# Kernel tuning notes

Hardware: AMD Instinct MI355X
Metric: run time of the kernel (lower is better)

## Reference

```python
import jax, jax.numpy as jnp
import numpy as np

B, S, D = 16, 1024, 768
H = 12
DH = D // H  # 64

def setup_inputs() -> dict:
    key = jax.random.key(0)
    ks = jax.random.split(key, 7)
    scale = 1.0 / np.sqrt(D)
    return {
        "hidden_states": jax.random.normal(ks[0], (B, S, D), dtype=jnp.float32),
        "Wq": jax.random.normal(ks[1], (D, D), dtype=jnp.float32) * scale,
        "bq": jnp.zeros((D,), dtype=jnp.float32),
        "Wk": jax.random.normal(ks[2], (D, D), dtype=jnp.float32) * scale,
        "bk": jnp.zeros((D,), dtype=jnp.float32),
        "Wv": jax.random.normal(ks[3], (D, D), dtype=jnp.float32) * scale,
        "bv": jnp.zeros((D,), dtype=jnp.float32),
    }

def reference(hidden_states, Wq, bq, Wk, bk, Wv, bv):
    # QKV projections: [B,S,D] -> [B,S,H,DH] -> [B,H,S,DH]
    def proj(W, b):
        y = hidden_states @ W.T + b
        return y.reshape(B, S, H, DH).transpose(0, 2, 1, 3)
    q = proj(Wq, bq)
    k = proj(Wk, bk)
    v = proj(Wv, bv)
    # attention scores [B,H,S,S], scaled by sqrt(d_head)
    scores = jnp.einsum('bhqd,bhkd->bhqk', q, k) / jnp.sqrt(jnp.float32(DH))
    probs = jax.nn.softmax(scores, axis=-1)
    # dropout prob = 0.0 (eval) -> identity
    ctx = jnp.einsum('bhqk,bhkd->bhqd', probs, v)
    ctx = ctx.transpose(0, 2, 1, 3).reshape(B, S, D)
    return ctx
```

## Files before the change

kernel.cpp:

```cpp
#include <hip/hip_runtime.h>
#include <hip/hip_bf16.h>

typedef __attribute__((ext_vector_type(8))) short short8;
typedef __attribute__((ext_vector_type(4))) float float4v;

#define MFMA_BF16 __builtin_amdgcn_mfma_f32_16x16x32_bf16

__device__ __forceinline__ unsigned short f2b(float f) {
  union { float f; unsigned u; } v; v.f = f;
  unsigned r = v.u + 0x7FFFu + ((v.u >> 16) & 1u);
  return (unsigned short)(r >> 16);
}

__device__ __forceinline__ unsigned pk2(float x, float y) {
  float2 v; v.x = x; v.y = y;
  __hip_bfloat162 h = __float22bfloat162_rn(v);
  union { __hip_bfloat162 h; unsigned u; } c; c.h = h;
  return c.u;
}

__device__ __forceinline__ void gld16(const unsigned short* g, unsigned short* l) {
  __builtin_amdgcn_global_load_lds(
      (const __attribute__((address_space(1))) unsigned int*)g,
      (__attribute__((address_space(3))) unsigned int*)l, 16, 0, 0);
}

__device__ __forceinline__ int swa(int r, int k) {
  return (r << 6) + ((((k >> 3) ^ r ^ (r >> 3)) & 7) << 3) + (k & 7);
}
__device__ __forceinline__ int swb(int r, int k) {
  return (r << 5) + ((((k >> 3) ^ r ^ (r >> 3)) & 3) << 3) + (k & 7);
}

__global__ __launch_bounds__(256) void cast_f32_bf16(const float* __restrict__ src,
                                                     unsigned short* __restrict__ dst,
                                                     int n4) {
  int i = blockIdx.x * 256 + threadIdx.x;
  if (i >= n4) return;
  float4 f = ((const float4*)src)[i];
  ushort4 o;
  o.x = f2b(f.x); o.y = f2b(f.y); o.z = f2b(f.z); o.w = f2b(f.w);
  ((ushort4*)dst)[i] = o;
}

__global__ __launch_bounds__(256) void cast_w3(const float* __restrict__ s0,
                                               const float* __restrict__ s1,
                                               const float* __restrict__ s2,
                                               unsigned short* __restrict__ dst) {
  const int z = blockIdx.y;
  const float* src = (z == 0) ? s0 : (z == 1 ? s1 : s2);
  int i = blockIdx.x * 256 + threadIdx.x;
  float4 f = ((const float4*)src)[i];
  ushort4 o;
  o.x = f2b(f.x); o.y = f2b(f.y); o.z = f2b(f.z); o.w = f2b(f.w);
  ((ushort4*)(dst + (size_t)z * 589824))[i] = o;
}

__global__ __launch_bounds__(256) void qkv_gemm(
    const unsigned short* __restrict__ X, const unsigned short* __restrict__ Wall,
    const float* __restrict__ b0, const float* __restrict__ b1, const float* __restrict__ b2,
    unsigned short* __restrict__ O0, unsigned short* __restrict__ O1, unsigned short* __restrict__ OVT) {
  __shared__ __align__(16) unsigned short Sh[16384];
  unsigned short* As = Sh;
  unsigned short* Bs = Sh + 8192;
  const int z = blockIdx.z;
  const unsigned short* W = Wall + (size_t)z * 589824;
  const float* bias = (z == 0) ? b0 : (z == 1 ? b1 : b2);
  const int m0 = blockIdx.x * 128, n0 = blockIdx.y * 128;
  const int t = threadIdx.x, w = t >> 6, l = t & 63, qd = l >> 4, col = l & 15;
  const int wm = (w & 1) * 64, wn = (w >> 1) * 64;

  float4v acc[4][4];
#pragma unroll
  for (int i = 0; i < 4; ++i)
#pragma unroll
    for (int j = 0; j < 4; ++j) acc[i][j] = (float4v)0.0f;

  const unsigned short* Xp = X + (size_t)m0 * 768;
  const unsigned short* Wp = W + (size_t)n0 * 768;

  for (int k0 = 0; k0 < 768; k0 += 64) {
#pragma unroll
    for (int p = 0; p < 4; ++p) {
      const int c = p * 256 + t;
      const int row = c >> 3;
      const int cc = (c ^ row ^ (row >> 3)) & 7;
      gld16(&Xp[(size_t)row * 768 + k0 + cc * 8], &As[c * 8]);
      gld16(&Wp[(size_t)row * 768 + k0 + cc * 8], &Bs[c * 8]);
    }
    __syncthreads();
#pragma unroll
    for (int ks = 0; ks < 2; ++ks) {
      short8 af[4], bf[4];
#pragma unroll
      for (int mi = 0; mi < 4; ++mi)
        af[mi] = *(const short8*)&As[swa(wm + mi * 16 + col, ks * 32 + qd * 8)];
#pragma unroll
      for (int ni = 0; ni < 4; ++ni)
        bf[ni] = *(const short8*)&Bs[swa(wn + ni * 16 + col, ks * 32 + qd * 8)];
#pragma unroll
      for (int mi = 0; mi < 4; ++mi)
#pragma unroll
        for (int ni = 0; ni < 4; ++ni)
          acc[mi][ni] = MFMA_BF16(af[mi], bf[ni], acc[mi][ni], 0, 0, 0);
    }
    __syncthreads();
  }

  if (z < 2) {
    unsigned short* O = (z == 0) ? O0 : O1;
#pragma unroll
    for (int ni = 0; ni < 4; ++ni) {
      const int n = n0 + wn + ni * 16 + col;
      const float bb = bias[n];
#pragma unroll
      for (int mi = 0; mi < 4; ++mi)
#pragma unroll
        for (int r = 0; r < 4; ++r) {
          const int m = m0 + wm + mi * 16 + qd * 4 + r;
          O[(size_t)m * 768 + n] = f2b(acc[mi][ni][r] + bb);
        }
    }
  } else {
#pragma unroll
    for (int ni = 0; ni < 4; ++ni) {
      const int nl = wn + ni * 16 + col;
      const float bb = bias[n0 + nl];
#pragma unroll
      for (int mi = 0; mi < 4; ++mi) {
        const int ml = wm + mi * 16 + qd * 4;
        ushort4 o;
        o.x = f2b(acc[mi][ni][0] + bb);
        o.y = f2b(acc[mi][ni][1] + bb);
        o.z = f2b(acc[mi][ni][2] + bb);
        o.w = f2b(acc[mi][ni][3] + bb);
        *(ushort4*)&Sh[(nl << 7) + ((((ml >> 3) ^ nl) & 15) << 3) + (ml & 7)] = o;
      }
    }
    __syncthreads();
    const int nl = t >> 1, mh = (t & 1) * 64;
    const int n = n0 + nl, hh = n >> 6, dd = n & 63;
    unsigned short* dstp =
        &OVT[(((size_t)(m0 >> 10) * 12 + hh) * 64 + dd) * 1024 + (m0 & 1023) + mh];
#pragma unroll
    for (int j = 0; j < 8; ++j) {
      const int mc = (mh >> 3) + j;
      uint4 vv = *(const uint4*)&Sh[(nl << 7) + (((mc ^ nl) & 15) << 3)];
      *(uint4*)&dstp[j * 8] = vv;
    }
  }
}

__global__ __launch_bounds__(256) void attn(
    const unsigned short* __restrict__ Q, const unsigned short* __restrict__ K,
    const unsigned short* __restrict__ VT, float* __restrict__ O) {
  __shared__ __align__(16) unsigned short Ks0[4096];
  __shared__ __align__(16) unsigned short Ks1[4096];
  __shared__ __align__(16) unsigned short Vt0[4096];
  __shared__ __align__(16) unsigned short Vt1[4096];
  __shared__ __align__(16) unsigned short Pls[4096];

  const int qt = blockIdx.x, h = blockIdx.y, b = blockIdx.z;
  const int t = threadIdx.x, w = t >> 6, l = t & 63, qd = l >> 4, col = l & 15;
  const size_t bh = (size_t)b * 786432 + (size_t)h * 64;
  const unsigned short* Kb = K + bh;
  const unsigned short* VTb = VT + ((size_t)(b * 12 + h)) * 65536;

  short8 qf[2][2];
  {
    const unsigned short* Qg = Q + bh + (size_t)(qt * 128 + w * 32) * 768;
#pragma unroll
    for (int mi = 0; mi < 2; ++mi)
#pragma unroll
      for (int ks = 0; ks < 2; ++ks)
        qf[mi][ks] =
            *(const short8*)&Qg[(size_t)(mi * 16 + col) * 768 + ks * 32 + qd * 8];
  }

  const int c0 = t, c1 = 256 + t;
  const int r0 = c0 >> 3, cc0 = (c0 ^ r0 ^ (r0 >> 3)) & 7;
  const int r1 = c1 >> 3, cc1 = (c1 ^ r1 ^ (r1 >> 3)) & 7;

#define STAGE_K(ktile, dst)                                             \
  do {                                                                  \
    const unsigned short* Kg_ = Kb + (size_t)(ktile)*49152;             \
    gld16(&Kg_[(size_t)r0 * 768 + cc0 * 8], &dst[c0 * 8]);              \
    gld16(&Kg_[(size_t)r1 * 768 + cc1 * 8], &dst[c1 * 8]);              \
  } while (0)

#define STAGE_V(ktile, dst)                                             \
  do {                                                                  \
    const unsigned short* Vg_ = VTb + (ktile)*64;                       \
    gld16(&Vg_[(size_t)r0 * 1024 + cc0 * 8], &dst[c0 * 8]);             \
    gld16(&Vg_[(size_t)r1 * 1024 + cc1 * 8], &dst[c1 * 8]);             \
  } while (0)

  STAGE_K(0, Ks0);
  STAGE_V(0, Vt0);

  float4v acc[2][4];
  float lrun[2] = {0.0f, 0.0f};
#pragma unroll
  for (int mi = 0; mi < 2; ++mi)
#pragma unroll
    for (int dt = 0; dt < 4; ++dt) acc[mi][dt] = (float4v)0.0f;

  const float LS = 0.18033688f;

  __syncthreads();

#define ATTN_ITER(kt, KsR, VtR, KsW, VtW)                                 \
  do {                                                                    \
    short8 kf[2][4];                                                      \
    _Pragma("unroll") for (int ks = 0; ks < 2; ++ks)                      \
        _Pragma("unroll") for (int ni = 0; ni < 4; ++ni)                  \
        kf[ks][ni] =                                                      \
        *(const short8*)&KsR[swa(ni * 16 + col, ks * 32 + qd * 8)];       \
    STAGE_K(((kt) + 1) & 15, KsW);                                        \
    STAGE_V(((kt) + 1) & 15, VtW);                                        \
    float4v sT[2][4];                                                     \
    _Pragma("unroll") for (int mi = 0; mi < 2; ++mi)                      \
        _Pragma("unroll") for (int ni = 0; ni < 4; ++ni)                  \
        sT[mi][ni] = (float4v)0.0f;                                       \
    _Pragma("unroll") for (int ks = 0; ks < 2; ++ks)                      \
        _Pragma("unroll") for (int ni = 0; ni < 4; ++ni) {                \
      sT[0][ni] = MFMA_BF16(kf[ks][ni], qf[0][ks], sT[0][ni], 0, 0, 0);   \
      sT[1][ni] = MFMA_BF16(kf[ks][ni], qf[1][ks], sT[1][ni], 0, 0, 0);   \
    }                                                                     \
    float rs0 = 0.0f, rs1 = 0.0f;                                         \
    _Pragma("unroll") for (int ks = 0; ks < 2; ++ks) {                    \
      _Pragma("unroll") for (int mi = 0; mi < 2; ++mi) {                  \
        const int row = w * 32 + mi * 16 + col;                           \
        _Pragma("unroll") for (int nl = 0; nl < 2; ++nl) {                \
          const int ni = ks * 2 + nl;                                     \
          float p0 = exp2f(LS * sT[mi][ni][0]);                           \
          float p1 = exp2f(LS * sT[mi][ni][1]);                           \
          float p2 = exp2f(LS * sT[mi][ni][2]);                           \
          float p3 = exp2f(LS * sT[mi][ni][3]);                           \
          if (mi == 0) rs0 += (p0 + p1) + (p2 + p3);                      \
          else         rs1 += (p0 + p1) + (p2 + p3);                      \
          union { unsigned u[2]; unsigned long long ull; } pk;            \
          pk.u[0] = pk2(p0, p1);                                          \
          pk.u[1] = pk2(p2, p3);                                          \
          *(unsigned long long*)&Pls[swb(row, nl * 16 + qd * 4)] = pk.ull;\
        }                                                                 \
      }                                                                   \
      const int kk = ks * 32 + qd * 8;                                    \
      short8 pf[2];                                                       \
      _Pragma("unroll") for (int mi = 0; mi < 2; ++mi)                    \
          pf[mi] = *(const short8*)&Pls[swb(w * 32 + mi * 16 + col, qd * 8)]; \
      _Pragma("unroll") for (int dt = 0; dt < 4; ++dt) {                  \
        short8 vf = *(const short8*)&VtR[swa(dt * 16 + col, kk)];         \
        acc[0][dt] = MFMA_BF16(vf, pf[0], acc[0][dt], 0, 0, 0);           \
        acc[1][dt] = MFMA_BF16(vf, pf[1], acc[1][dt], 0, 0, 0);           \
      }                                                                   \
    }                                                                     \
    lrun[0] += rs0;                                                       \
    lrun[1] += rs1;                                                       \
    __syncthreads();                                                      \
  } while (0)

  for (int kt2 = 0; kt2 < 16; kt2 += 2) {
    ATTN_ITER(kt2, Ks0, Vt0, Ks1, Vt1);
    ATTN_ITER(kt2 + 1, Ks1, Vt1, Ks0, Vt0);
  }

#pragma unroll
  for (int mi = 0; mi < 2; ++mi) {
    lrun[mi] += __shfl_xor(lrun[mi], 16);
    lrun[mi] += __shfl_xor(lrun[mi], 32);
  }
  float* Og = O + (size_t)(b * 1024 + qt * 128) * 768 + h * 64;
#pragma unroll
  for (int mi = 0; mi < 2; ++mi) {
    const float rl = 1.0f / lrun[mi];
    const int q = w * 32 + mi * 16 + col;
#pragma unroll
    for (int dt = 0; dt < 4; ++dt) {
      float4 o;
      o.x = acc[mi][dt][0] * rl;
      o.y = acc[mi][dt][1] * rl;
      o.z = acc[mi][dt][2] * rl;
      o.w = acc[mi][dt][3] * rl;
      *(float4*)&Og[(size_t)q * 768 + dt * 16 + qd * 4] = o;
    }
  }
#undef STAGE_K
#undef STAGE_V
#undef ATTN_ITER
}

extern "C" void kernel_launch(void* const* d_in, const int* in_sizes, int n_in,
                              void* d_out, int out_size, void* d_ws, size_t ws_size,
                              hipStream_t stream) {
  const float* hs = (const float*)d_in[0];
  const float* Wq = (const float*)d_in[1];
  const float* bq = (const float*)d_in[2];
  const float* Wk = (const float*)d_in[3];
  const float* bk = (const float*)d_in[4];
  const float* Wv = (const float*)d_in[5];
  const float* bv = (const float*)d_in[6];
  float* out = (float*)d_out;
  char* ws = (char*)d_ws;

  unsigned short* Xb = (unsigned short*)ws;
  unsigned short* Wb = (unsigned short*)(ws + 25165824);
  unsigned short* Qb = (unsigned short*)(ws + 28704768);
  unsigned short* Kb = (unsigned short*)(ws + 53870592);
  unsigned short* Vb = (unsigned short*)(ws + 79036416);

  cast_f32_bf16<<<12288, 256, 0, stream>>>(hs, Xb, 3145728);
  cast_w3<<<dim3(576, 3), 256, 0, stream>>>(Wq, Wk, Wv, Wb);

  qkv_gemm<<<dim3(128, 6, 3), 256, 0, stream>>>(Xb, Wb, bq, bk, bv, Qb, Kb, Vb);

  attn<<<dim3(8, 12, 16), 256, 0, stream>>>(Qb, Kb, Vb, out);
}
```

Measured before the change: 312.0 us.

## Keep softmax probabilities in registers via permlane swaps and fold scale into Q

The attention kernel no longer writes probabilities to LDS and reads them back. Exponentiated scores are packed to bf16 and rearranged into MFMA operand layout with permlane32/permlane16 swaps, and row sums come from an extra MFMA against a ones vector instead of shuffles. The softmax scale is folded into the Q projection epilogue, and exp2 uses the raw hardware intrinsic. Other changes: next-tile staging moves before the K fragment reads and skips the redundant wraparound load, the grid becomes 1D with a remapped block order for L2 locality, and the casts use packed bf16 conversion. Risks include rounding differences from the scaled Q in bf16, and the permlane lane mapping has to match the MFMA operand layout exactly.

```diff
diff --git a/kernel.cpp b/kernel.cpp
--- a/kernel.cpp
+++ b/kernel.cpp
@@ -3,6 +3,7 @@
 
 typedef __attribute__((ext_vector_type(8))) short short8;
 typedef __attribute__((ext_vector_type(4))) float float4v;
+typedef __attribute__((ext_vector_type(2))) unsigned int uint2v;
 
 #define MFMA_BF16 __builtin_amdgcn_mfma_f32_16x16x32_bf16
 
@@ -27,9 +28,6 @@
 
 __device__ __forceinline__ int swa(int r, int k) {
   return (r << 6) + ((((k >> 3) ^ r ^ (r >> 3)) & 7) << 3) + (k & 7);
-}
-__device__ __forceinline__ int swb(int r, int k) {
-  return (r << 5) + ((((k >> 3) ^ r ^ (r >> 3)) & 3) << 3) + (k & 7);
 }
 
 __global__ __launch_bounds__(256) void cast_f32_bf16(const float* __restrict__ src,
@@ -38,9 +36,10 @@
   int i = blockIdx.x * 256 + threadIdx.x;
   if (i >= n4) return;
   float4 f = ((const float4*)src)[i];
-  ushort4 o;
-  o.x = f2b(f.x); o.y = f2b(f.y); o.z = f2b(f.z); o.w = f2b(f.w);
-  ((ushort4*)dst)[i] = o;
+  uint2 o;
+  o.x = pk2(f.x, f.y);
+  o.y = pk2(f.z, f.w);
+  ((uint2*)dst)[i] = o;
 }
 
 __global__ __launch_bounds__(256) void cast_w3(const float* __restrict__ s0,
@@ -51,9 +50,10 @@
   const float* src = (z == 0) ? s0 : (z == 1 ? s1 : s2);
   int i = blockIdx.x * 256 + threadIdx.x;
   float4 f = ((const float4*)src)[i];
-  ushort4 o;
-  o.x = f2b(f.x); o.y = f2b(f.y); o.z = f2b(f.z); o.w = f2b(f.w);
-  ((ushort4*)(dst + (size_t)z * 589824))[i] = o;
+  uint2 o;
+  o.x = pk2(f.x, f.y);
+  o.y = pk2(f.z, f.w);
+  ((uint2*)(dst + (size_t)z * 589824))[i] = o;
 }
 
 __global__ __launch_bounds__(256) void qkv_gemm(
@@ -109,6 +109,7 @@
 
   if (z < 2) {
     unsigned short* O = (z == 0) ? O0 : O1;
+    const float osc = (z == 0) ? 0.18033688f : 1.0f;
 #pragma unroll
     for (int ni = 0; ni < 4; ++ni) {
       const int n = n0 + wn + ni * 16 + col;
@@ -118,7 +119,7 @@
 #pragma unroll
         for (int r = 0; r < 4; ++r) {
           const int m = m0 + wm + mi * 16 + qd * 4 + r;
-          O[(size_t)m * 768 + n] = f2b(acc[mi][ni][r] + bb);
+          O[(size_t)m * 768 + n] = f2b((acc[mi][ni][r] + bb) * osc);
         }
     }
   } else {
@@ -158,9 +159,14 @@
   __shared__ __align__(16) unsigned short Ks1[4096];
   __shared__ __align__(16) unsigned short Vt0[4096];
   __shared__ __align__(16) unsigned short Vt1[4096];
-  __shared__ __align__(16) unsigned short Pls[4096];
-
-  const int qt = blockIdx.x, h = blockIdx.y, b = blockIdx.z;
+
+  const int g = blockIdx.x;
+  const int orig = (g & 7) * 192 + (g >> 3);
+  const int qt = orig & 7;
+  const int hb = orig >> 3;
+  const int b = hb / 12;
+  const int h = hb - b * 12;
+
   const int t = threadIdx.x, w = t >> 6, l = t & 63, qd = l >> 4, col = l & 15;
   const size_t bh = (size_t)b * 786432 + (size_t)h * 64;
   const unsigned short* Kb = K + bh;
@@ -199,25 +205,31 @@
   STAGE_V(0, Vt0);
 
   float4v acc[2][4];
-  float lrun[2] = {0.0f, 0.0f};
-#pragma unroll
-  for (int mi = 0; mi < 2; ++mi)
+  float4v accl[2];
+#pragma unroll
+  for (int mi = 0; mi < 2; ++mi) {
+    accl[mi] = (float4v)0.0f;
 #pragma unroll
     for (int dt = 0; dt < 4; ++dt) acc[mi][dt] = (float4v)0.0f;
-
-  const float LS = 0.18033688f;
+  }
+
+  short8 ones;
+#pragma unroll
+  for (int j = 0; j < 8; ++j) ones[j] = (short)0x3F80;
 
   __syncthreads();
 
 #define ATTN_ITER(kt, KsR, VtR, KsW, VtW)                                 \
   do {                                                                    \
+    if ((kt) < 15) {                                                      \
+      STAGE_K((kt) + 1, KsW);                                             \
+      STAGE_V((kt) + 1, VtW);                                             \
+    }                                                                     \
     short8 kf[2][4];                                                      \
     _Pragma("unroll") for (int ks = 0; ks < 2; ++ks)                      \
         _Pragma("unroll") for (int ni = 0; ni < 4; ++ni)                  \
         kf[ks][ni] =                                                      \
         *(const short8*)&KsR[swa(ni * 16 + col, ks * 32 + qd * 8)];       \
-    STAGE_K(((kt) + 1) & 15, KsW);                                        \
-    STAGE_V(((kt) + 1) & 15, VtW);                                        \
     float4v sT[2][4];                                                     \
     _Pragma("unroll") for (int mi = 0; mi < 2; ++mi)                      \
         _Pragma("unroll") for (int ni = 0; ni < 4; ++ni)                  \
@@ -227,36 +239,38 @@
       sT[0][ni] = MFMA_BF16(kf[ks][ni], qf[0][ks], sT[0][ni], 0, 0, 0);   \
       sT[1][ni] = MFMA_BF16(kf[ks][ni], qf[1][ks], sT[1][ni], 0, 0, 0);   \
     }                                                                     \
-    float rs0 = 0.0f, rs1 = 0.0f;                                         \
-    _Pragma("unroll") for (int ks = 0; ks < 2; ++ks) {                    \
+    _Pragma("unroll") for (int s = 0; s < 2; ++s) {                       \
+      short8 pf[2];                                                       \
       _Pragma("unroll") for (int mi = 0; mi < 2; ++mi) {                  \
-        const int row = w * 32 + mi * 16 + col;                           \
-        _Pragma("unroll") for (int nl = 0; nl < 2; ++nl) {                \
-          const int ni = ks * 2 + nl;                                     \
-          float p0 = exp2f(LS * sT[mi][ni][0]);                           \
-          float p1 = exp2f(LS * sT[mi][ni][1]);                           \
-          float p2 = exp2f(LS * sT[mi][ni][2]);                           \
-          float p3 = exp2f(LS * sT[mi][ni][3]);                           \
-          if (mi == 0) rs0 += (p0 + p1) + (p2 + p3);                      \
-          else         rs1 += (p0 + p1) + (p2 + p3);                      \
-          union { unsigned u[2]; unsigned long long ull; } pk;            \
-          pk.u[0] = pk2(p0, p1);                                          \
-          pk.u[1] = pk2(p2, p3);                                          \
-          *(unsigned long long*)&Pls[swb(row, nl * 16 + qd * 4)] = pk.ull;\
-        }                                                                 \
+        float4v sa = sT[mi][s * 2 + 0];                                   \
+        float4v sb = sT[mi][s * 2 + 1];                                   \
+        unsigned A0 = pk2(__builtin_amdgcn_exp2f(sa[0]),                  \
+                          __builtin_amdgcn_exp2f(sa[1]));                 \
+        unsigned A1 = pk2(__builtin_amdgcn_exp2f(sa[2]),                  \
+                          __builtin_amdgcn_exp2f(sa[3]));                 \
+        unsigned B0 = pk2(__builtin_amdgcn_exp2f(sb[0]),                  \
+                          __builtin_amdgcn_exp2f(sb[1]));                 \
+        unsigned B1 = pk2(__builtin_amdgcn_exp2f(sb[2]),                  \
+                          __builtin_amdgcn_exp2f(sb[3]));                 \
+         \
+        uint2v x0 = __builtin_amdgcn_permlane32_swap(A0, B0, false, false);   \
+        uint2v x1 = __builtin_amdgcn_permlane32_swap(A1, B1, false, false);   \
+        uint2v y02 = __builtin_amdgcn_permlane16_swap(x0[0], x0[1], false, false); \
+        uint2v y13 = __builtin_amdgcn_permlane16_swap(x1[0], x1[1], false, false); \
+        union { unsigned u[4]; short8 v; } pu;                            \
+        pu.u[0] = y02[0]; pu.u[1] = y13[0];                               \
+        pu.u[2] = y02[1]; pu.u[3] = y13[1];                               \
+        pf[mi] = pu.v;                                                    \
       }                                                                   \
-      const int kk = ks * 32 + qd * 8;                                    \
-      short8 pf[2];                                                       \
-      _Pragma("unroll") for (int mi = 0; mi < 2; ++mi)                    \
-          pf[mi] = *(const short8*)&Pls[swb(w * 32 + mi * 16 + col, qd * 8)]; \
+      const int kk = s * 32 + qd * 8;                                     \
       _Pragma("unroll") for (int dt = 0; dt < 4; ++dt) {                  \
         short8 vf = *(const short8*)&VtR[swa(dt * 16 + col, kk)];         \
         acc[0][dt] = MFMA_BF16(vf, pf[0], acc[0][dt], 0, 0, 0);           \
         acc[1][dt] = MFMA_BF16(vf, pf[1], acc[1][dt], 0, 0, 0);           \
       }                                                                   \
+      accl[0] = MFMA_BF16(ones, pf[0], accl[0], 0, 0, 0);                 \
+      accl[1] = MFMA_BF16(ones, pf[1], accl[1], 0, 0, 0);                 \
     }                                                                     \
-    lrun[0] += rs0;                                                       \
-    lrun[1] += rs1;                                                       \
     __syncthreads();                                                      \
   } while (0)
 
@@ -265,15 +279,10 @@
     ATTN_ITER(kt2 + 1, Ks1, Vt1, Ks0, Vt0);
   }
 
+  float* Og = O + (size_t)(b * 1024 + qt * 128) * 768 + h * 64;
 #pragma unroll
   for (int mi = 0; mi < 2; ++mi) {
-    lrun[mi] += __shfl_xor(lrun[mi], 16);
-    lrun[mi] += __shfl_xor(lrun[mi], 32);
-  }
-  float* Og = O + (size_t)(b * 1024 + qt * 128) * 768 + h * 64;
-#pragma unroll
-  for (int mi = 0; mi < 2; ++mi) {
-    const float rl = 1.0f / lrun[mi];
+    const float rl = 1.0f / accl[mi][0];
     const int q = w * 32 + mi * 16 + col;
 #pragma unroll
     for (int dt = 0; dt < 4; ++dt) {
@@ -314,5 +323,5 @@
 
   qkv_gemm<<<dim3(128, 6, 3), 256, 0, stream>>>(Xb, Wb, bq, bk, bv, Qb, Kb, Vb);
 
-  attn<<<dim3(8, 12, 16), 256, 0, stream>>>(Qb, Kb, Vb, out);
-}
+  attn<<<dim3(1536), 256, 0, stream>>>(Qb, Kb, Vb, out);
+}
```

Measured after the change: 273.1 us. -12.4%, faster.
